# Kernel optimization log

Hardware: AMD Instinct MI355X
Metric: run time of the kernel (lower is better)

The kernel has to match this reference:

```python
import jax, jax.numpy as jnp
import numpy as np

N, T, F = 64, 256, 13          # nodes/frame, frames, node features
E = N * (N - 1)                 # complete directed graph (as in _extract_graph)
P, HID, HEADS = 128, 128, 4     # pooling_channels, hidden_dim, attention_heads


def setup_inputs() -> dict:
    key = jax.random.key(0)
    ks = jax.random.split(key, 32)
    s = 0.05
    src, dst = np.nonzero(~np.eye(N, dtype=bool))
    edge_index = jnp.array(np.stack([src, dst]), dtype=jnp.int32)
    C1 = P // HEADS
    rn = lambda k, shp: jax.random.normal(k, shp, jnp.float32) * s
    return {
        "x": jax.random.normal(ks[0], (T, N, F), jnp.float32),
        "edge_index": edge_index,
        "edge_attr": jax.random.uniform(ks[1], (T, E, 1), jnp.float32),
        # GATConv 1: in=F, heads=4, per-head C1, edge_dim=1, concat -> P
        "W1": rn(ks[2], (F, P)),
        "a_src1": rn(ks[3], (HEADS, C1)),
        "a_dst1": rn(ks[4], (HEADS, C1)),
        "We1": rn(ks[5], (1, P)),
        "a_edge1": rn(ks[6], (HEADS, C1)),
        "b1": jnp.zeros((P,), jnp.float32),
        # GATConv 2: in=P, heads=1, out=HID
        "W2": rn(ks[7], (P, HID)),
        "a_src2": rn(ks[8], (1, HID)),
        "a_dst2": rn(ks[9], (1, HID)),
        "We2": rn(ks[10], (1, HID)),
        "a_edge2": rn(ks[11], (1, HID)),
        "b2": jnp.zeros((HID,), jnp.float32),
        # AttentionalAggregation gate: Linear(HID, 1)
        "Wg": rn(ks[12], (HID, 1)),
        "bg": jnp.zeros((1,), jnp.float32),
        # bidirectional LSTM: input 2*HID, hidden HID (torch gate order i,f,g,o)
        "Wih_f": rn(ks[13], (4 * HID, 2 * HID)),
        "Whh_f": rn(ks[14], (4 * HID, HID)),
        "bih_f": jnp.zeros((4 * HID,), jnp.float32),
        "bhh_f": jnp.zeros((4 * HID,), jnp.float32),
        "Wih_b": rn(ks[15], (4 * HID, 2 * HID)),
        "Whh_b": rn(ks[16], (4 * HID, HID)),
        "bih_b": jnp.zeros((4 * HID,), jnp.float32),
        "bhh_b": jnp.zeros((4 * HID,), jnp.float32),
        # output layer: Linear(2*HID, 1)
        "Wo": rn(ks[17], (2 * HID, 1)),
        "bo": jnp.zeros((1,), jnp.float32),
    }


def reference(x, edge_index, edge_attr, W1, a_src1, a_dst1, We1, a_edge1, b1,
              W2, a_src2, a_dst2, We2, a_edge2, b2, Wg, bg,
              Wih_f, Whh_f, bih_f, bhh_f, Wih_b, Whh_b, bih_b, bhh_b, Wo, bo):
    n = x.shape[1]
    src, dst = edge_index[0], edge_index[1]

    def gat(h_in, ea, W, a_s, a_d, We, a_e, b):
        # PyG GATConv with edge_dim, add_self_loops=False, eval (no dropout)
        heads = a_s.shape[0]
        hc = W.shape[1]
        c = hc // heads
        h = (h_in @ W).reshape(-1, heads, c)          # [N, H, C]
        e = (ea @ We).reshape(-1, heads, c)           # [E, H, C]
        alpha = (h * a_s).sum(-1)[src] + (h * a_d).sum(-1)[dst] + (e * a_e).sum(-1)
        alpha = jax.nn.leaky_relu(alpha, 0.2)         # [E, H]
        amax = jax.ops.segment_max(alpha, dst, num_segments=n)
        amax = jnp.where(jnp.isfinite(amax), amax, 0.0)
        ex = jnp.exp(alpha - amax[dst])
        den = jax.ops.segment_sum(ex, dst, num_segments=n)
        coef = ex / (den[dst] + 1e-16)                # softmax per dst node
        out = jax.ops.segment_sum(h[src] * coef[:, :, None], dst, num_segments=n)
        return out.reshape(n, hc) + b

    def gnn(xt, eat):
        h1 = jax.nn.relu(gat(xt, eat, W1, a_src1, a_dst1, We1, a_edge1, b1))
        h2 = jax.nn.relu(gat(h1, eat, W2, a_src2, a_dst2, We2, a_edge2, b2))
        attn = jax.nn.softmax(h2 @ Wg + bg, axis=0)   # AttentionalAggregation
        return jnp.concatenate([(attn * h2).sum(0), h2.max(0)])  # [2*HID]

    embs = jax.vmap(gnn)(x, edge_attr)                # [T, 2*HID]

    def lstm(Wih, Whh, bih, bhh, seq):
        hid = Whh.shape[1]
        def step(carry, xt):
            h, c = carry
            g = xt @ Wih.T + h @ Whh.T + bih + bhh
            i, f, gg, o = jnp.split(g, 4)
            c = jax.nn.sigmoid(f) * c + jax.nn.sigmoid(i) * jnp.tanh(gg)
            h = jax.nn.sigmoid(o) * jnp.tanh(c)
            return (h, c), h
        init = (jnp.zeros((hid,), seq.dtype), jnp.zeros((hid,), seq.dtype))
        _, outs = jax.lax.scan(step, init, seq)
        return outs

    outs_f = lstm(Wih_f, Whh_f, bih_f, bhh_f, embs)
    outs_b = lstm(Wih_b, Whh_b, bih_b, bhh_b, embs[::-1])
    # lstm_out[:, -1, :] = [fwd state at t=T-1, bwd state at t=T-1]
    last = jnp.concatenate([outs_f[-1], outs_b[0]])
    return jax.nn.sigmoid(last @ Wo + bo)[None, :]    # [1, 1]
```

## Files before the change

### kernel.cpp

```cpp
#include <hip/hip_runtime.h>
#include <math.h>

#define NN 64
#define TT 256
#define FF 13
#define EE 4032
#define PP 128
#define HH 128

typedef float f32x4 __attribute__((ext_vector_type(4)));
typedef _Float16 f16x2 __attribute__((ext_vector_type(2)));

__device__ __forceinline__ float wave_sum64(float v) {
#pragma unroll
  for (int off = 32; off > 0; off >>= 1) v += __shfl_xor(v, off, 64);
  return v;
}
__device__ __forceinline__ float sigm(float x) { return 1.f / (1.f + __expf(-x)); }
__device__ __forceinline__ float tanh_fast(float x) { return 1.f - 2.f / (__expf(2.f * x) + 1.f); }

#define ROTF(x, N) __builtin_bit_cast(float, __builtin_amdgcn_mov_dpp( \
    __builtin_bit_cast(int, x), 0x120 + (N), 0xF, 0xF, true))
__device__ __forceinline__ float rdlane(float v, int l) {
  return __builtin_bit_cast(float, __builtin_amdgcn_readlane(__builtin_bit_cast(int, v), l));
}
__device__ __forceinline__ float allred_max(float v) {
  v = fmaxf(v, ROTF(v, 1)); v = fmaxf(v, ROTF(v, 2));
  v = fmaxf(v, ROTF(v, 4)); v = fmaxf(v, ROTF(v, 8));
  return fmaxf(fmaxf(rdlane(v, 0), rdlane(v, 16)),
               fmaxf(rdlane(v, 32), rdlane(v, 48)));
}
__device__ __forceinline__ float allred_sum(float v) {
  v += ROTF(v, 1); v += ROTF(v, 2); v += ROTF(v, 4); v += ROTF(v, 8);
  return (rdlane(v, 0) + rdlane(v, 16)) + (rdlane(v, 32) + rdlane(v, 48));
}

__device__ __forceinline__ unsigned pk_f16(float lo, float hi) {
  unsigned u;
  asm("v_cvt_pkrtz_f16_f32 %0, %1, %2" : "=v"(u) : "v"(lo), "v"(hi));
  return u;
}
__device__ __forceinline__ float fdot2u(unsigned h, unsigned w, float acc) {
#if __has_builtin(__builtin_amdgcn_fdot2)
  return __builtin_amdgcn_fdot2(__builtin_bit_cast(f16x2, h),
                                __builtin_bit_cast(f16x2, w), acc, false);
#else
  const f16x2 a = __builtin_bit_cast(f16x2, h);
  const f16x2 b = __builtin_bit_cast(f16x2, w);
  return acc + (float)a.x * (float)b.x + (float)a.y * (float)b.y;
#endif
}
__device__ __forceinline__ float ror1(float x) {
  return __builtin_bit_cast(float, __builtin_amdgcn_mov_dpp(
      __builtin_bit_cast(int, x), 0x121, 0xF, 0xF, true));
}
__device__ __forceinline__ float qswap1(float x) {
  return __builtin_bit_cast(float, __builtin_amdgcn_mov_dpp(
      __builtin_bit_cast(int, x), 0xB1, 0xF, 0xF, true));
}

__global__ __launch_bounds__(512, 2)
void gnn_kernel(const float* __restrict__ x, const float* __restrict__ ea_g,
                const float* __restrict__ W1, const float* __restrict__ a_src1,
                const float* __restrict__ a_dst1, const float* __restrict__ We1,
                const float* __restrict__ a_edge1, const float* __restrict__ b1,
                const float* __restrict__ W2, const float* __restrict__ a_src2,
                const float* __restrict__ a_dst2, const float* __restrict__ We2,
                const float* __restrict__ a_edge2, const float* __restrict__ b2,
                const float* __restrict__ Wg, const float* __restrict__ bg,
                float* __restrict__ embs)
{
  __shared__ float x_s[NN * FF];
  __shared__ float W1_s[FF * PP];
  __shared__ float ea_s[EE];
  __shared__ float hA_s[NN * PP];
  __shared__ float hB_s[NN * PP];
  __shared__ float as1_s[4 * NN];
  __shared__ float ad1_s[4 * NN];
  __shared__ float asrc1_s[PP], adst1_s[PP], asrc2_s[PP], adst2_s[PP];
  __shared__ float b1_s[PP], b2_s[PP], Wg_s[PP];
  __shared__ float as2_s[NN], ad2_s[NN];
  __shared__ __align__(16) float coefA_s[16 * 272];
  __shared__ float denA_s[16 * 4];
  __shared__ __align__(16) float coefB_s[16 * 68];
  __shared__ float denB_s[16];
  __shared__ float wed_s[8];
  __shared__ float attn_s[NN];

  const int tid = threadIdx.x;
  const int t = blockIdx.x;
  const int wave = tid >> 6, lane = tid & 63;

  for (int i = tid; i < NN * FF; i += 512) x_s[i] = x[t * NN * FF + i];
  for (int i = tid; i < FF * PP; i += 512) W1_s[i] = W1[i];
  for (int i = tid; i < EE; i += 512) ea_s[i] = ea_g[t * EE + i];
  if (tid < PP) {
    asrc1_s[tid] = a_src1[tid]; adst1_s[tid] = a_dst1[tid];
    asrc2_s[tid] = a_src2[tid]; adst2_s[tid] = a_dst2[tid];
    b1_s[tid] = b1[tid]; b2_s[tid] = b2[tid]; Wg_s[tid] = Wg[tid];
  }
  if (tid >= 128 && tid < 132) {
    const int h = tid - 128;
    float acc = 0.f;
    for (int c = 0; c < 32; ++c) acc += We1[h * 32 + c] * a_edge1[h * 32 + c];
    wed_s[h] = acc;
  }
  if (tid == 132) {
    float acc = 0.f;
    for (int c = 0; c < 128; ++c) acc += We2[c] * a_edge2[c];
    wed_s[4] = acc;
  }
  __syncthreads();

  {
    const int c = tid & 127, ib = tid >> 7;
    for (int q = 0; q < 16; ++q) {
      const int i = ib * 16 + q;
      float acc = 0.f;
#pragma unroll
      for (int f = 0; f < FF; ++f) acc += x_s[i * FF + f] * W1_s[f * PP + c];
      hA_s[i * PP + c] = acc;
    }
  }
  __syncthreads();

  {
    const int half = tid >> 8;
    const int tt2 = tid & 255;
    const int i = tt2 >> 2, h = tt2 & 3;
    const float* aw = half ? adst1_s : asrc1_s;
    float acc = 0.f;
    for (int cc = 0; cc < 32; ++cc) {
      const int c = (cc + tid) & 31;
      acc += hA_s[i * PP + h * 32 + c] * aw[h * 32 + c];
    }
    if (half) ad1_s[h * 64 + i] = acc; else as1_s[h * 64 + i] = acc;
  }
  __syncthreads();

  for (int g = 0; g < 4; ++g) {
#pragma unroll
    for (int r = 0; r < 2; ++r) {
      const int d = g * 16 + r * 8 + wave;
      const int dl = d & 15;
      float a0, a1, a2, a3;
      if (lane != d) {
        const int jj = lane * 63 + (d < lane ? d : d - 1);
        const float ev = ea_s[jj];
        a0 = as1_s[0 * 64 + lane] + ad1_s[0 * 64 + d] + ev * wed_s[0];
        a1 = as1_s[1 * 64 + lane] + ad1_s[1 * 64 + d] + ev * wed_s[1];
        a2 = as1_s[2 * 64 + lane] + ad1_s[2 * 64 + d] + ev * wed_s[2];
        a3 = as1_s[3 * 64 + lane] + ad1_s[3 * 64 + d] + ev * wed_s[3];
        a0 = a0 > 0.f ? a0 : 0.2f * a0;
        a1 = a1 > 0.f ? a1 : 0.2f * a1;
        a2 = a2 > 0.f ? a2 : 0.2f * a2;
        a3 = a3 > 0.f ? a3 : 0.2f * a3;
      } else { a0 = a1 = a2 = a3 = -1e30f; }
      const float m0 = allred_max(a0), m1 = allred_max(a1);
      const float m2 = allred_max(a2), m3 = allred_max(a3);
      const float p0 = (lane != d) ? __expf(a0 - m0) : 0.f;
      const float p1 = (lane != d) ? __expf(a1 - m1) : 0.f;
      const float p2 = (lane != d) ? __expf(a2 - m2) : 0.f;
      const float p3 = (lane != d) ? __expf(a3 - m3) : 0.f;
      const float s0 = allred_sum(p0), s1 = allred_sum(p1);
      const float s2 = allred_sum(p2), s3 = allred_sum(p3);
      coefA_s[dl * 272 + 0 * 68 + lane] = p0;
      coefA_s[dl * 272 + 1 * 68 + lane] = p1;
      coefA_s[dl * 272 + 2 * 68 + lane] = p2;
      coefA_s[dl * 272 + 3 * 68 + lane] = p3;
      if (lane == 0) {
        denA_s[dl * 4 + 0] = s0; denA_s[dl * 4 + 1] = s1;
        denA_s[dl * 4 + 2] = s2; denA_s[dl * 4 + 3] = s3;
      }
    }
    __syncthreads();
    {
      const int half = lane >> 5;
      const int dl = wave * 2 + half;
      const int d  = g * 16 + dl;
      const int c0 = (lane & 31) * 4;
      const int hh = c0 >> 5;
      const float* cfb = &coefA_s[dl * 272 + hh * 68];
      float ac0 = 0.f, ac1 = 0.f, ac2 = 0.f, ac3 = 0.f;
#pragma unroll 4
      for (int s = 0; s < 64; s += 4) {
        const float4 cf = *(const float4*)&cfb[s];
        const float4 h0 = *(const float4*)&hA_s[(s + 0) * PP + c0];
        ac0 += cf.x * h0.x; ac1 += cf.x * h0.y; ac2 += cf.x * h0.z; ac3 += cf.x * h0.w;
        const float4 h1v = *(const float4*)&hA_s[(s + 1) * PP + c0];
        ac0 += cf.y * h1v.x; ac1 += cf.y * h1v.y; ac2 += cf.y * h1v.z; ac3 += cf.y * h1v.w;
        const float4 h2v = *(const float4*)&hA_s[(s + 2) * PP + c0];
        ac0 += cf.z * h2v.x; ac1 += cf.z * h2v.y; ac2 += cf.z * h2v.z; ac3 += cf.z * h2v.w;
        const float4 h3v = *(const float4*)&hA_s[(s + 3) * PP + c0];
        ac0 += cf.w * h3v.x; ac1 += cf.w * h3v.y; ac2 += cf.w * h3v.z; ac3 += cf.w * h3v.w;
      }
      const float inv = 1.f / (denA_s[dl * 4 + hh] + 1e-16f);
      const float4 bv = *(const float4*)&b1_s[c0];
      float4 o;
      o.x = fmaxf(ac0 * inv + bv.x, 0.f);
      o.y = fmaxf(ac1 * inv + bv.y, 0.f);
      o.z = fmaxf(ac2 * inv + bv.z, 0.f);
      o.w = fmaxf(ac3 * inv + bv.w, 0.f);
      *(float4*)&hB_s[d * PP + c0] = o;
    }
    __syncthreads();
  }

  {
    const int cg = tid & 31, ig = tid >> 5;
    const int c0 = cg * 4, i0 = ig * 4;
    float acc[4][4];
#pragma unroll
    for (int ii = 0; ii < 4; ++ii)
#pragma unroll
      for (int cc = 0; cc < 4; ++cc) acc[ii][cc] = 0.f;
    for (int f0 = 0; f0 < 128; f0 += 4) {
      float4 wv0 = *(const float4*)&W2[(f0 + 0) * PP + c0];
      float4 wv1 = *(const float4*)&W2[(f0 + 1) * PP + c0];
      float4 wv2 = *(const float4*)&W2[(f0 + 2) * PP + c0];
      float4 wv3 = *(const float4*)&W2[(f0 + 3) * PP + c0];
#pragma unroll
      for (int ii = 0; ii < 4; ++ii) {
        const float4 hv = *(const float4*)&hB_s[(i0 + ii) * PP + f0];
        acc[ii][0] += hv.x * wv0.x + hv.y * wv1.x + hv.z * wv2.x + hv.w * wv3.x;
        acc[ii][1] += hv.x * wv0.y + hv.y * wv1.y + hv.z * wv2.y + hv.w * wv3.y;
        acc[ii][2] += hv.x * wv0.z + hv.y * wv1.z + hv.z * wv2.z + hv.w * wv3.z;
        acc[ii][3] += hv.x * wv0.w + hv.y * wv1.w + hv.z * wv2.w + hv.w * wv3.w;
      }
    }
#pragma unroll
    for (int ii = 0; ii < 4; ++ii) {
      float4 o; o.x = acc[ii][0]; o.y = acc[ii][1]; o.z = acc[ii][2]; o.w = acc[ii][3];
      *(float4*)&hA_s[(i0 + ii) * PP + c0] = o;
    }
  }
  __syncthreads();

  if (tid < 128) {
    const int i = tid >> 1, sel = tid & 1;
    const float* aw = sel ? adst2_s : asrc2_s;
    float acc = 0.f;
    for (int cc = 0; cc < 128; ++cc) {
      const int c = (cc + tid) & 127;
      acc += hA_s[i * PP + c] * aw[c];
    }
    if (sel) ad2_s[i] = acc; else as2_s[i] = acc;
  }
  __syncthreads();

  for (int g = 0; g < 4; ++g) {
#pragma unroll
    for (int r = 0; r < 2; ++r) {
      const int d = g * 16 + r * 8 + wave;
      const int dl = d & 15;
      float a;
      if (lane != d) {
        const int jj = lane * 63 + (d < lane ? d : d - 1);
        a = as2_s[lane] + ad2_s[d] + ea_s[jj] * wed_s[4];
        a = a > 0.f ? a : 0.2f * a;
      } else a = -1e30f;
      const float m = allred_max(a);
      const float p = (lane != d) ? __expf(a - m) : 0.f;
      const float ssum = allred_sum(p);
      coefB_s[dl * 68 + lane] = p;
      if (lane == 0) denB_s[dl] = ssum;
    }
    __syncthreads();
    {
      const int half = lane >> 5;
      const int dl = wave * 2 + half;
      const int d  = g * 16 + dl;
      const int c0 = (lane & 31) * 4;
      const float* cfb = &coefB_s[dl * 68];
      float ac0 = 0.f, ac1 = 0.f, ac2 = 0.f, ac3 = 0.f;
#pragma unroll 4
      for (int s = 0; s < 64; s += 4) {
        const float4 cf = *(const float4*)&cfb[s];
        const float4 h0 = *(const float4*)&hA_s[(s + 0) * PP + c0];
        ac0 += cf.x * h0.x; ac1 += cf.x * h0.y; ac2 += cf.x * h0.z; ac3 += cf.x * h0.w;
        const float4 h1v = *(const float4*)&hA_s[(s + 1) * PP + c0];
        ac0 += cf.y * h1v.x; ac1 += cf.y * h1v.y; ac2 += cf.y * h1v.z; ac3 += cf.y * h1v.w;
        const float4 h2v = *(const float4*)&hA_s[(s + 2) * PP + c0];
        ac0 += cf.z * h2v.x; ac1 += cf.z * h2v.y; ac2 += cf.z * h2v.z; ac3 += cf.z * h2v.w;
        const float4 h3v = *(const float4*)&hA_s[(s + 3) * PP + c0];
        ac0 += cf.w * h3v.x; ac1 += cf.w * h3v.y; ac2 += cf.w * h3v.z; ac3 += cf.w * h3v.w;
      }
      const float inv = 1.f / (denB_s[dl] + 1e-16f);
      const float4 bv = *(const float4*)&b2_s[c0];
      float4 o;
      o.x = fmaxf(ac0 * inv + bv.x, 0.f);
      o.y = fmaxf(ac1 * inv + bv.y, 0.f);
      o.z = fmaxf(ac2 * inv + bv.z, 0.f);
      o.w = fmaxf(ac3 * inv + bv.w, 0.f);
      *(float4*)&hB_s[d * PP + c0] = o;
    }
    __syncthreads();
  }

  if (tid < 64) {
    float acc = 0.f;
    for (int cc = 0; cc < 128; ++cc) {
      const int c = (cc + tid) & 127;
      acc += hB_s[tid * PP + c] * Wg_s[c];
    }
    const float logit = acc + bg[0];
    const float m = allred_max(logit);
    const float p = __expf(logit - m);
    const float ssum = allred_sum(p);
    attn_s[tid] = p / ssum;
  }
  __syncthreads();
  if (tid < 128) {
    const int c = tid;
    float acc = 0.f, mx = -1e30f;
    for (int i = 0; i < NN; ++i) {
      const float v = hB_s[i * PP + c];
      acc += attn_s[i] * v;
      mx = fmaxf(mx, v);
    }
    embs[t * 256 + c] = acc;
    embs[t * 256 + 128 + c] = mx;
  }
}

__global__ __launch_bounds__(512, 2)
void zproj_kernel(const float* __restrict__ embs,
                  const float* __restrict__ Wih_f, const float* __restrict__ bih_f,
                  const float* __restrict__ bhh_f,
                  const float* __restrict__ Wih_b, const float* __restrict__ bih_b,
                  const float* __restrict__ bhh_b,
                  float* __restrict__ Z, float* __restrict__ Zb)
{
  __shared__ float e_s[256];
  const int t = blockIdx.x;
  const int j = threadIdx.x;
  const bool bwd = (t == TT);
  const int tsrc = bwd ? (TT - 1) : t;
  if (j < 256) e_s[j] = embs[tsrc * 256 + j];
  __syncthreads();
  const float* W = bwd ? Wih_b : Wih_f;
  float acc = bwd ? (bih_b[j] + bhh_b[j]) : (bih_f[j] + bhh_f[j]);
  const float4* Wr = (const float4*)(W + j * 256);
  const float4* er = (const float4*)e_s;
#pragma unroll 8
  for (int k = 0; k < 64; ++k) {
    const float4 w = Wr[k];
    const float4 e = er[k];
    acc += w.x * e.x + w.y * e.y + w.z * e.z + w.w * e.w;
  }
  if (bwd) Zb[j] = acc; else Z[t * 512 + j] = acc;
}

__global__ __launch_bounds__(1024)
void lstm_kernel(const float* __restrict__ Z, const float* __restrict__ Zb,
                 const float* __restrict__ Whh_f,
                 const float* __restrict__ Wo, const float* __restrict__ bo,
                 float* __restrict__ out)
{
  __shared__ float g_s[512];
  __shared__ __align__(16) unsigned h16_s[64];
  __shared__ float h_s[128];
  __shared__ float hb_s[128];
  __shared__ float red_s[16];
  const int tid = threadIdx.x;
  const int wave = tid >> 6, lane = tid & 63;
  const int m = lane & 15;
  const int s = lane >> 5;
  const int gbase = wave * 32 + ((lane >> 4) & 1) * 16;
  const int j = wave * 32 + (lane & 31);

  const float* wbase = Whh_f + s * 64 + 4 * m;
#define LWR(r) \
  unsigned wa##r, wb##r; { \
    const float4 v = *(const float4*)(wbase + (gbase + ((m - (r)) & 15)) * 128); \
    wa##r = pk_f16(v.x, v.y); wb##r = pk_f16(v.z, v.w); }
  LWR(0)  LWR(1)  LWR(2)  LWR(3)  LWR(4)  LWR(5)  LWR(6)  LWR(7)
  LWR(8)  LWR(9)  LWR(10) LWR(11) LWR(12) LWR(13) LWR(14) LWR(15)
#undef LWR
  asm volatile("" : "+v"(wa0),  "+v"(wb0),  "+v"(wa1),  "+v"(wb1),
                    "+v"(wa2),  "+v"(wb2),  "+v"(wa3),  "+v"(wb3),
                    "+v"(wa4),  "+v"(wb4),  "+v"(wa5),  "+v"(wb5),
                    "+v"(wa6),  "+v"(wb6),  "+v"(wa7),  "+v"(wb7));
  asm volatile("" : "+v"(wa8),  "+v"(wb8),  "+v"(wa9),  "+v"(wb9),
                    "+v"(wa10), "+v"(wb10), "+v"(wa11), "+v"(wb11),
                    "+v"(wa12), "+v"(wb12), "+v"(wa13), "+v"(wb13),
                    "+v"(wa14), "+v"(wb14), "+v"(wa15), "+v"(wb15));

  float c = 0.f;
  if (tid < 128) h_s[tid] = 0.f;
  if (tid < 64) h16_s[tid] = 0u;
  __syncthreads();

  float zcur = Z[j];
  for (int t = 0; t < TT; ++t) {
    const float znext = (t < TT - 1) ? Z[(t + 1) * 512 + j] : 0.f;
    const uint2 hd = *(const uint2*)&h16_s[s * 32 + 2 * m];
    float acc = 0.f;
#define STEP(r) \
    acc = fdot2u(hd.x, wa##r, acc); \
    acc = fdot2u(hd.y, wb##r, acc); \
    acc = ror1(acc);
    STEP(0)  STEP(1)  STEP(2)  STEP(3)  STEP(4)  STEP(5)  STEP(6)  STEP(7)
    STEP(8)  STEP(9)  STEP(10) STEP(11) STEP(12) STEP(13) STEP(14) STEP(15)
#undef STEP
    const float full = acc + __shfl_xor(acc, 32, 64);
    if (lane < 32) g_s[j] = full + zcur;
    __syncthreads();
    if (tid < 128) {
      const float gi = g_s[tid], gf = g_s[128 + tid];
      const float gg = g_s[256 + tid], go = g_s[384 + tid];
      const float ei = __expf(-gi), ef = __expf(-gf);
      const float eo = __expf(-go), eg = __expf(2.f * gg);
      const float si = 1.f / (1.f + ei), sf = 1.f / (1.f + ef);
      const float so = 1.f / (1.f + eo);
      const float tg = 1.f - 2.f / (eg + 1.f);
      c = sf * c + si * tg;
      const float ec = __expf(2.f * c);
      const float hnew = so * (1.f - 2.f / (ec + 1.f));
      h_s[tid] = hnew;
      const float hnb = qswap1(hnew);
      if (!(tid & 1)) h16_s[tid >> 1] = pk_f16(hnew, hnb);
    }
    __syncthreads();
    zcur = znext;
  }

  if (tid < 128) {
    const float gi = Zb[tid], gg = Zb[256 + tid], go = Zb[384 + tid];
    const float cb = sigm(gi) * tanh_fast(gg);
    hb_s[tid] = sigm(go) * tanh_fast(cb);
  }
  __syncthreads();

  float v = 0.f;
  if (tid < 128) v = h_s[tid] * Wo[tid];
  else if (tid < 256) v = hb_s[tid - 128] * Wo[tid];
  v = wave_sum64(v);
  if ((tid & 63) == 0) red_s[tid >> 6] = v;
  __syncthreads();
  if (tid == 0) {
    float sum = bo[0];
#pragma unroll
    for (int k = 0; k < 16; ++k) sum += red_s[k];
    out[0] = 1.f / (1.f + __expf(-sum));
  }
}

extern "C" void kernel_launch(void* const* d_in, const int* in_sizes, int n_in,
                              void* d_out, int out_size, void* d_ws, size_t ws_size,
                              hipStream_t stream) {
  const float* x       = (const float*)d_in[0];
  const float* ea      = (const float*)d_in[2];
  const float* W1      = (const float*)d_in[3];
  const float* a_src1  = (const float*)d_in[4];
  const float* a_dst1  = (const float*)d_in[5];
  const float* We1     = (const float*)d_in[6];
  const float* a_edge1 = (const float*)d_in[7];
  const float* b1      = (const float*)d_in[8];
  const float* W2      = (const float*)d_in[9];
  const float* a_src2  = (const float*)d_in[10];
  const float* a_dst2  = (const float*)d_in[11];
  const float* We2     = (const float*)d_in[12];
  const float* a_edge2 = (const float*)d_in[13];
  const float* b2      = (const float*)d_in[14];
  const float* Wg      = (const float*)d_in[15];
  const float* bg      = (const float*)d_in[16];
  const float* Wih_f   = (const float*)d_in[17];
  const float* Whh_f   = (const float*)d_in[18];
  const float* bih_f   = (const float*)d_in[19];
  const float* bhh_f   = (const float*)d_in[20];
  const float* Wih_b   = (const float*)d_in[21];
  const float* bih_b   = (const float*)d_in[23];
  const float* bhh_b   = (const float*)d_in[24];
  const float* Wo      = (const float*)d_in[25];
  const float* bo      = (const float*)d_in[26];
  float* out = (float*)d_out;

  float* embs = (float*)d_ws;
  float* Z    = embs + 256 * 256;
  float* Zb   = Z + 256 * 512;

  gnn_kernel<<<256, 512, 0, stream>>>(x, ea, W1, a_src1, a_dst1, We1, a_edge1, b1,
                                      W2, a_src2, a_dst2, We2, a_edge2, b2, Wg, bg, embs);
  zproj_kernel<<<257, 512, 0, stream>>>(embs, Wih_f, bih_f, bhh_f, Wih_b, bih_b, bhh_b, Z, Zb);
  lstm_kernel<<<1, 1024, 0, stream>>>(Z, Zb, Whh_f, Wo, bo, out);
}
```

Before: 271.4 us.

## Interleave LSTM gate rows per lane to fuse cell update and drop a barrier

Reassigns the Whh rows held by each lane so the four gates (i,f,g,o) of one hidden unit sit in adjacent lanes of a DPP quad. The gate nonlinearities and the cell update are then computed in registers via quad broadcasts, with no shared-memory gate buffer. The h vector is double-buffered in shared memory, which cuts the per-timestep barriers from two to one on the serial recurrence. In exchange every lane now evaluates activations redundantly, and the gate/row mapping and pair-packing shift must be exactly right.

```diff
diff --git a/kernel.cpp b/kernel.cpp
--- a/kernel.cpp
+++ b/kernel.cpp
@@ -54,9 +54,25 @@
   return __builtin_bit_cast(float, __builtin_amdgcn_mov_dpp(
       __builtin_bit_cast(int, x), 0x121, 0xF, 0xF, true));
 }
-__device__ __forceinline__ float qswap1(float x) {
+__device__ __forceinline__ float qb0(float x) {
   return __builtin_bit_cast(float, __builtin_amdgcn_mov_dpp(
-      __builtin_bit_cast(int, x), 0xB1, 0xF, 0xF, true));
+      __builtin_bit_cast(int, x), 0x00, 0xF, 0xF, true));
+}
+__device__ __forceinline__ float qb1(float x) {
+  return __builtin_bit_cast(float, __builtin_amdgcn_mov_dpp(
+      __builtin_bit_cast(int, x), 0x55, 0xF, 0xF, true));
+}
+__device__ __forceinline__ float qb2(float x) {
+  return __builtin_bit_cast(float, __builtin_amdgcn_mov_dpp(
+      __builtin_bit_cast(int, x), 0xAA, 0xF, 0xF, true));
+}
+__device__ __forceinline__ float qb3(float x) {
+  return __builtin_bit_cast(float, __builtin_amdgcn_mov_dpp(
+      __builtin_bit_cast(int, x), 0xFF, 0xF, 0xF, true));
+}
+__device__ __forceinline__ float shr4(float x) {
+  return __builtin_bit_cast(float, __builtin_amdgcn_mov_dpp(
+      __builtin_bit_cast(int, x), 0x114, 0xF, 0xF, true));
 }
 
 __global__ __launch_bounds__(512, 2)
@@ -357,8 +373,7 @@
                  const float* __restrict__ Wo, const float* __restrict__ bo,
                  float* __restrict__ out)
 {
-  __shared__ float g_s[512];
-  __shared__ __align__(16) unsigned h16_s[64];
+  __shared__ __align__(16) unsigned h16_s[2][64];
   __shared__ float h_s[128];
   __shared__ float hb_s[128];
   __shared__ float red_s[16];
@@ -366,13 +381,14 @@
   const int wave = tid >> 6, lane = tid & 63;
   const int m = lane & 15;
   const int s = lane >> 5;
-  const int gbase = wave * 32 + ((lane >> 4) & 1) * 16;
-  const int j = wave * 32 + (lane & 31);
-
+  const int ub = wave * 8 + ((lane >> 4) & 1) * 4;
+  const int gt = lane & 3;
+
+#define ROWQ(q) (((((q) & 3)) << 7) + ub + ((q) >> 2))
   const float* wbase = Whh_f + s * 64 + 4 * m;
 #define LWR(r) \
   unsigned wa##r, wb##r; { \
-    const float4 v = *(const float4*)(wbase + (gbase + ((m - (r)) & 15)) * 128); \
+    const float4 v = *(const float4*)(wbase + ROWQ((m - (r)) & 15) * 128); \
     wa##r = pk_f16(v.x, v.y); wb##r = pk_f16(v.z, v.w); }
   LWR(0)  LWR(1)  LWR(2)  LWR(3)  LWR(4)  LWR(5)  LWR(6)  LWR(7)
   LWR(8)  LWR(9)  LWR(10) LWR(11) LWR(12) LWR(13) LWR(14) LWR(15)
@@ -386,15 +402,17 @@
                     "+v"(wa12), "+v"(wb12), "+v"(wa13), "+v"(wb13),
                     "+v"(wa14), "+v"(wb14), "+v"(wa15), "+v"(wb15));
 
+  const int myrow = ROWQ(m);
   float c = 0.f;
-  if (tid < 128) h_s[tid] = 0.f;
-  if (tid < 64) h16_s[tid] = 0u;
-  __syncthreads();
-
-  float zcur = Z[j];
+  float h = 0.f;
+  if (tid < 64) { h16_s[0][tid] = 0u; }
+  __syncthreads();
+
+  float zcur = Z[myrow];
+  int p = 0;
   for (int t = 0; t < TT; ++t) {
-    const float znext = (t < TT - 1) ? Z[(t + 1) * 512 + j] : 0.f;
-    const uint2 hd = *(const uint2*)&h16_s[s * 32 + 2 * m];
+    const float znext = (t < TT - 1) ? Z[(t + 1) * 512 + myrow] : 0.f;
+    const uint2 hd = *(const uint2*)&h16_s[p][s * 32 + 2 * m];
     float acc = 0.f;
 #define STEP(r) \
     acc = fdot2u(hd.x, wa##r, acc); \
@@ -403,27 +421,22 @@
     STEP(0)  STEP(1)  STEP(2)  STEP(3)  STEP(4)  STEP(5)  STEP(6)  STEP(7)
     STEP(8)  STEP(9)  STEP(10) STEP(11) STEP(12) STEP(13) STEP(14) STEP(15)
 #undef STEP
-    const float full = acc + __shfl_xor(acc, 32, 64);
-    if (lane < 32) g_s[j] = full + zcur;
+    const float g = acc + __shfl_xor(acc, 32, 64) + zcur;
+    const float pre = (gt == 2) ? 2.f * g : g;
+    const float sv = 1.f / (1.f + __expf(-pre));
+    const float act = (gt == 2) ? 2.f * sv - 1.f : sv;
+    const float si = qb0(act), sf = qb1(act), tg = qb2(act), so = qb3(act);
+    c = sf * c + si * tg;
+    h = so * tanh_fast(c);
+    const float hnb = shr4(h);
+    if (lane < 32 && (lane & 7) == 0)
+      h16_s[p ^ 1][wave * 4 + (lane >> 3)] = pk_f16(h, hnb);
     __syncthreads();
-    if (tid < 128) {
-      const float gi = g_s[tid], gf = g_s[128 + tid];
-      const float gg = g_s[256 + tid], go = g_s[384 + tid];
-      const float ei = __expf(-gi), ef = __expf(-gf);
-      const float eo = __expf(-go), eg = __expf(2.f * gg);
-      const float si = 1.f / (1.f + ei), sf = 1.f / (1.f + ef);
-      const float so = 1.f / (1.f + eo);
-      const float tg = 1.f - 2.f / (eg + 1.f);
-      c = sf * c + si * tg;
-      const float ec = __expf(2.f * c);
-      const float hnew = so * (1.f - 2.f / (ec + 1.f));
-      h_s[tid] = hnew;
-      const float hnb = qswap1(hnew);
-      if (!(tid & 1)) h16_s[tid >> 1] = pk_f16(hnew, hnb);
-    }
-    __syncthreads();
+    p ^= 1;
     zcur = znext;
   }
+
+  if (lane < 32 && gt == 0) h_s[ub + ((lane & 15) >> 2)] = h;
 
   if (tid < 128) {
     const float gi = Zb[tid], gg = Zb[256 + tid], go = Zb[384 + tid];
```

New measurement: 283.5 us. 1.04x slower.
